# Optimization experiments

Measured on AMD Instinct MI355X. Metric: run time of the kernel, lower is better.

Reference implementation:

```python
import jax, jax.numpy as jnp
import numpy as np

N_NODES = 20000

def _gcn_conv(x, W, b, src, dst, n):
    # PyG GCNConv: add self-loops, symmetric normalization D^-1/2 (A+I) D^-1/2, then XW + b
    h = x @ W                                   # [n, out]
    loop = jnp.arange(n, dtype=src.dtype)
    s = jnp.concatenate([src, loop])            # sources incl. self-loops
    d = jnp.concatenate([dst, loop])            # targets incl. self-loops
    deg = jax.ops.segment_sum(jnp.ones_like(d, dtype=h.dtype), d, num_segments=n)
    dinv = jnp.where(deg > 0, jax.lax.rsqrt(deg), 0.0)
    norm = dinv[s] * dinv[d]                    # [E+n]
    msg = h[s] * norm[:, None]                  # gather + scale
    out = jax.ops.segment_sum(msg, d, num_segments=n)  # scatter-add
    return out + b


def setup_inputs() -> dict:
    key = jax.random.key(0)
    ks = jax.random.split(key, 12)
    n, text_dim, hidden, ncls = N_NODES, 768, 128, 4
    mel_flat = 128 * 128
    E = 640000
    def lin(k, fan_in, fan_out):
        bound = 1.0 / np.sqrt(fan_in)
        kw, kb = jax.random.split(k)
        W = jax.random.uniform(kw, (fan_in, fan_out), jnp.float32, -bound, bound)
        b = jax.random.uniform(kb, (fan_out,), jnp.float32, -bound, bound)
        return W, b
    W_mel, b_mel = lin(ks[0], mel_flat, hidden)
    W_cat, b_cat = lin(ks[1], text_dim + hidden, hidden)
    W1, b1 = lin(ks[2], hidden, hidden)
    W2, b2 = lin(ks[3], hidden, ncls)
    return {
        "text": jax.random.normal(ks[4], (n, text_dim), jnp.float32),
        "mel": jax.random.normal(ks[5], (n, 128, 128), jnp.float32),
        "edge_index": jax.random.randint(ks[6], (2, E), 0, n, jnp.int32),
        "W_mel": W_mel, "b_mel": b_mel,
        "W_cat": W_cat, "b_cat": b_cat,
        "W1": W1, "b1": b1,
        "W2": W2, "b2": b2,
    }


def reference(text, mel, edge_index, W_mel, b_mel, W_cat, b_cat, W1, b1, W2, b2):
    n = text.shape[0]
    src, dst = edge_index[0], edge_index[1]
    m = mel.reshape(n, -1)                      # flatten [N, 128*128]
    m = jax.nn.relu(m @ W_mel + b_mel)          # [N, hidden]
    x = jnp.concatenate([text, m], axis=1)      # [N, text_dim + hidden]
    x = jax.nn.relu(x @ W_cat + b_cat)          # [N, hidden]
    x = jax.nn.relu(_gcn_conv(x, W1, b1, src, dst, n))
    x = _gcn_conv(x, W2, b2, src, dst, n)       # [N, num_classes]
    return x
```

## Files before the change

### kernel.cpp

```cpp
#include <hip/hip_runtime.h>
#include <hip/hip_bf16.h>
#include <cstdint>

typedef float f32x4 __attribute__((ext_vector_type(4)));
typedef __bf16 bf16x8 __attribute__((ext_vector_type(8)));
typedef __bf16 bf16x4 __attribute__((ext_vector_type(4)));
typedef __bf16 bf16x2 __attribute__((ext_vector_type(2)));

#define HID 128

__global__ void pack_all(const float* __restrict__ Wa, const float* __restrict__ Wb,
                         const float* __restrict__ Wc,
                         __bf16* __restrict__ Ba, __bf16* __restrict__ Bb,
                         __bf16* __restrict__ Bc) {
    int idx = blockIdx.x * 256 + threadIdx.x;
    const int T1 = 512 * 512;
    const int T2 = 28 * 512;
    const int T3 = 4 * 512;
    const float* W; __bf16* B; int li;
    if (idx < T1)            { W = Wa; B = Ba; li = idx; }
    else if (idx < T1 + T2)  { W = Wb; B = Bb; li = idx - T1; }
    else if (idx < T1 + T2 + T3) { W = Wc; B = Bc; li = idx - T1 - T2; }
    else return;
    int lane = li & 63;
    int nf = (li >> 6) & 7;
    int ki = li >> 9;
    int n = nf * 16 + (lane & 15);
    int kb = ki * 32 + ((lane >> 4) * 8);
    bf16x8 v;
#pragma unroll
    for (int j = 0; j < 8; ++j) v[j] = (__bf16)W[(size_t)(kb + j) * HID + n];
    *reinterpret_cast<bf16x8*>(B + (size_t)li * 8) = v;
}

__global__ __launch_bounds__(256, 2) void gemm_mel_ks(
    const float* __restrict__ A0,
    const __bf16* __restrict__ Bf,
    float* __restrict__ part)
{
    const int tid = threadIdx.x;
    const int lane = tid & 63;
    const int wv = tid >> 6;
    const int quarter = blockIdx.x / 625;
    const int row_base = (blockIdx.x - quarter * 625) * 32;
    const int rif = lane & 15;
    const int kg = lane >> 4;
    const int s0 = quarter * 8;

    __shared__ __align__(16) char ldsb[65536];

    f32x4 zero = {0.f, 0.f, 0.f, 0.f};
    f32x4 acc[2][8];
#pragma unroll
    for (int i = 0; i < 2; ++i)
#pragma unroll
        for (int j = 0; j < 8; ++j) acc[i][j] = zero;

    const bf16x8* __restrict__ BfV = reinterpret_cast<const bf16x8*>(Bf);

    f32x4 st[16];

    auto stage_load = [&](int s) {
#pragma unroll
        for (int j = 0; j < 16; ++j) {
            int seg = wv * 16 + j;
            int row = seg >> 1, halfseg = seg & 1;
            const float* gp = A0 + (size_t)(row_base + row) * 16384 + s * 512 + halfseg * 256 + (lane << 2);
            st[j] = __builtin_nontemporal_load(reinterpret_cast<const f32x4*>(gp));
        }
    };
    auto stage_write = [&](int buf) {
#pragma unroll
        for (int j = 0; j < 16; ++j) {
            int seg = wv * 16 + j;
            int row = seg >> 1, halfseg = seg & 1;
            int byte = row * 1024 + ((halfseg * 512 + lane * 8) ^ ((row & 7) << 4)) + buf * 32768;
            bf16x4 v;
            v[0] = (__bf16)st[j][0]; v[1] = (__bf16)st[j][1];
            v[2] = (__bf16)st[j][2]; v[3] = (__bf16)st[j][3];
            *reinterpret_cast<bf16x4*>(ldsb + byte) = v;
        }
    };
    auto compute2 = [&](int cur, int s, int kt0) {
#pragma unroll
        for (int kt = kt0; kt < kt0 + 2; ++kt) {
            bf16x8 af[2];
#pragma unroll
            for (int mi = 0; mi < 2; ++mi) {
                int row = mi * 16 + rif;
                int byte = row * 1024 + ((wv * 256 + kt * 64 + kg * 16) ^ ((rif & 7) << 4)) + cur * 32768;
                af[mi] = *reinterpret_cast<const bf16x8*>(ldsb + byte);
            }
            int ki = s * 16 + wv * 4 + kt;
            const bf16x8* bp = BfV + (size_t)ki * 512 + lane;
#pragma unroll
            for (int nf = 0; nf < 8; ++nf) {
                bf16x8 b = bp[nf * 64];
                acc[0][nf] = __builtin_amdgcn_mfma_f32_16x16x32_bf16(af[0], b, acc[0][nf], 0, 0, 0);
                acc[1][nf] = __builtin_amdgcn_mfma_f32_16x16x32_bf16(af[1], b, acc[1][nf], 0, 0, 0);
            }
        }
    };

    stage_load(s0);
    stage_write(0);
    for (int t = 0; t < 8; ++t) {
        int s = s0 + t;
        int cur = t & 1;
        if (t + 1 < 8) stage_load(s + 1);
        __syncthreads();
        compute2(cur, s, 0);
        compute2(cur, s, 2);
        if (t + 1 < 8) stage_write(cur ^ 1);
    }

    __syncthreads();
    float* red = reinterpret_cast<float*>(ldsb);
#pragma unroll
    for (int mi = 0; mi < 2; ++mi)
#pragma unroll
        for (int nf = 0; nf < 8; ++nf)
#pragma unroll
            for (int j = 0; j < 4; ++j)
                red[(wv * 32 + mi * 16 + kg * 4 + j) * HID + nf * 16 + rif] = acc[mi][nf][j];
    __syncthreads();
    float* pb = part + (size_t)quarter * 20000 * HID;
#pragma unroll
    for (int p = 0; p < 16; ++p) {
        int idx = tid + p * 256;
        int r = idx >> 7, c = idx & 127;
        float v = red[r * HID + c] + red[(32 + r) * HID + c]
                + red[(64 + r) * HID + c] + red[(96 + r) * HID + c];
        pb[(size_t)(row_base + r) * HID + c] = v;
    }
}

__global__ void combine_m(const float* __restrict__ part, const float* __restrict__ bias,
                          __bf16* __restrict__ m) {
    int idx = blockIdx.x * 256 + threadIdx.x;
    const size_t N = (size_t)20000 * HID / 4;
    const f32x4* p = reinterpret_cast<const f32x4*>(part);
    f32x4 b = *reinterpret_cast<const f32x4*>(bias + (idx & 31) * 4);
    f32x4 v = p[idx] + p[idx + N] + p[idx + 2 * N] + p[idx + 3 * N] + b;
    bf16x4 r;
    r[0] = (__bf16)fmaxf(v.x, 0.f); r[1] = (__bf16)fmaxf(v.y, 0.f);
    r[2] = (__bf16)fmaxf(v.z, 0.f); r[3] = (__bf16)fmaxf(v.w, 0.f);
    *reinterpret_cast<bf16x4*>(m + (size_t)idx * 4) = r;
}

__global__ __launch_bounds__(256) void gemm_cat_h1(
    const float* __restrict__ A0,
    const __bf16* __restrict__ A1,
    const __bf16* __restrict__ Bf2,
    const __bf16* __restrict__ Bf3,
    const float* __restrict__ bcat,
    const float* __restrict__ dinv,
    __bf16* __restrict__ h1)
{
    const int tid = threadIdx.x;
    const int lane = tid & 63;
    const int w = tid >> 6;
    const int row_base = blockIdx.x * 32;
    const int rif = lane & 15;
    const int kg = lane >> 4;

    f32x4 zero = {0.f, 0.f, 0.f, 0.f};
    f32x4 acc[2][8];
#pragma unroll
    for (int i = 0; i < 2; ++i)
#pragma unroll
        for (int j = 0; j < 8; ++j) acc[i][j] = zero;

    const bf16x8* __restrict__ Bf2V = reinterpret_cast<const bf16x8*>(Bf2);
    const int kstart = w * 224;

#pragma unroll
    for (int it = 0; it < 7; ++it) {
        const int k0 = kstart + it * 32;
        const int kc = k0 + kg * 8;
        bf16x8 af[2];
#pragma unroll
        for (int mi = 0; mi < 2; ++mi) {
            const int row = row_base + mi * 16 + rif;
            if (k0 < 768) {
                const f32x4* apv = reinterpret_cast<const f32x4*>(A0 + (size_t)row * 768 + kc);
                f32x4 v0 = __builtin_nontemporal_load(apv);
                f32x4 v1 = __builtin_nontemporal_load(apv + 1);
                af[mi][0] = (__bf16)v0.x; af[mi][1] = (__bf16)v0.y;
                af[mi][2] = (__bf16)v0.z; af[mi][3] = (__bf16)v0.w;
                af[mi][4] = (__bf16)v1.x; af[mi][5] = (__bf16)v1.y;
                af[mi][6] = (__bf16)v1.z; af[mi][7] = (__bf16)v1.w;
            } else {
                af[mi] = *reinterpret_cast<const bf16x8*>(A1 + (size_t)row * HID + (kc - 768));
            }
        }
        const bf16x8* bp = Bf2V + (size_t)(k0 >> 5) * 512 + lane;
#pragma unroll
        for (int nf = 0; nf < 8; ++nf) {
            bf16x8 b = bp[nf * 64];
            acc[0][nf] = __builtin_amdgcn_mfma_f32_16x16x32_bf16(af[0], b, acc[0][nf], 0, 0, 0);
            acc[1][nf] = __builtin_amdgcn_mfma_f32_16x16x32_bf16(af[1], b, acc[1][nf], 0, 0, 0);
        }
    }

    __shared__ float red[4][32][HID];
    __shared__ __bf16 xs[32][136];

#pragma unroll
    for (int mi = 0; mi < 2; ++mi)
#pragma unroll
        for (int nf = 0; nf < 8; ++nf)
#pragma unroll
            for (int j = 0; j < 4; ++j)
                red[w][mi * 16 + kg * 4 + j][nf * 16 + rif] = acc[mi][nf][j];
    __syncthreads();
#pragma unroll
    for (int p = 0; p < 16; ++p) {
        int idx = tid + p * 256;
        int r = idx >> 7, c = idx & 127;
        float v = red[0][r][c] + red[1][r][c] + red[2][r][c] + red[3][r][c];
        v = fmaxf(v + bcat[c], 0.f);
        xs[r][c] = (__bf16)v;
    }
    __syncthreads();

    f32x4 acc2[2][8];
#pragma unroll
    for (int i = 0; i < 2; ++i)
#pragma unroll
        for (int j = 0; j < 8; ++j) acc2[i][j] = zero;

    {
        const int k0 = w * 32;
        bf16x8 af[2];
#pragma unroll
        for (int mi = 0; mi < 2; ++mi)
            af[mi] = *reinterpret_cast<const bf16x8*>(&xs[mi * 16 + rif][k0 + kg * 8]);
        const bf16x8* bp = reinterpret_cast<const bf16x8*>(Bf3) + (size_t)w * 512 + lane;
#pragma unroll
        for (int nf = 0; nf < 8; ++nf) {
            bf16x8 b = bp[nf * 64];
            acc2[0][nf] = __builtin_amdgcn_mfma_f32_16x16x32_bf16(af[0], b, acc2[0][nf], 0, 0, 0);
            acc2[1][nf] = __builtin_amdgcn_mfma_f32_16x16x32_bf16(af[1], b, acc2[1][nf], 0, 0, 0);
        }
    }

#pragma unroll
    for (int mi = 0; mi < 2; ++mi)
#pragma unroll
        for (int nf = 0; nf < 8; ++nf)
#pragma unroll
            for (int j = 0; j < 4; ++j)
                red[w][mi * 16 + kg * 4 + j][nf * 16 + rif] = acc2[mi][nf][j];
    __syncthreads();
#pragma unroll
    for (int p = 0; p < 16; ++p) {
        int idx = tid + p * 256;
        int r = idx >> 7, c = idx & 127;
        float v = red[0][r][c] + red[1][r][c] + red[2][r][c] + red[3][r][c];
        h1[(size_t)(row_base + r) * HID + c] = (__bf16)(v * dinv[row_base + r]);
    }
}

__global__ void count_dst(const int* __restrict__ dst, int* __restrict__ cnt, int E) {
    int e = blockIdx.x * 256 + threadIdx.x;
    if (e < E) atomicAdd(&cnt[dst[e]], 1);
}

__global__ __launch_bounds__(1024) void scan_block(const int* __restrict__ cnt,
    int* __restrict__ offs, float* __restrict__ dinv, int n) {
    int tid = threadIdx.x;
    int CH = (n + 1023) >> 10;
    int s0 = tid * CH;
    int s1 = min(s0 + CH, n);
    int sum = 0;
    for (int i = s0; i < s1; ++i) sum += cnt[i];
    int lane = tid & 63, wv = tid >> 6;
    int s = sum;
#pragma unroll
    for (int off = 1; off < 64; off <<= 1) {
        int t = __shfl_up(s, off);
        if (lane >= off) s += t;
    }
    __shared__ int wsum[16];
    __shared__ int wbase[16];
    if (lane == 63) wsum[wv] = s;
    __syncthreads();
    if (tid == 0) {
        int a = 0;
#pragma unroll
        for (int k = 0; k < 16; ++k) { wbase[k] = a; a += wsum[k]; }
    }
    __syncthreads();
    int run = wbase[wv] + (s - sum);
    for (int i = s0; i < s1; ++i) {
        int v = cnt[i];
        offs[i] = run;
        dinv[i] = rsqrtf((float)(v + 1));
        run += v;
    }
}

__global__ void fill_csr(const int* __restrict__ src, const int* __restrict__ dst,
                         const int* __restrict__ offs, int* __restrict__ fill,
                         int* __restrict__ srcs, int E) {
    int e = blockIdx.x * 256 + threadIdx.x;
    if (e >= E) return;
    int d = dst[e];
    int p = offs[d] + atomicAdd(&fill[d], 1);
    srcs[p] = src[e];
}

__global__ __launch_bounds__(64) void agg_h_w2(const __bf16* __restrict__ hs,
    const float* __restrict__ dinv, const int* __restrict__ offs,
    const int* __restrict__ cnt, const int* __restrict__ srcs,
    const float* __restrict__ b1, const float* __restrict__ W2,
    float* __restrict__ h2, int n) {
    int i = blockIdx.x;
    int c = threadIdx.x;
    float di = dinv[i];
    const int col = 2 * c;
    bf16x2 hv = *reinterpret_cast<const bf16x2*>(hs + (size_t)i * HID + col);
    float a0 = (float)hv[0];
    float a1 = (float)hv[1];
    int o = offs[i], e = cnt[i];
    int t = 0;
    for (; t + 4 <= e; t += 4) {
        int s0 = srcs[o + t], s1 = srcs[o + t + 1], s2 = srcs[o + t + 2], s3 = srcs[o + t + 3];
        bf16x2 v0 = *reinterpret_cast<const bf16x2*>(hs + (size_t)s0 * HID + col);
        bf16x2 v1 = *reinterpret_cast<const bf16x2*>(hs + (size_t)s1 * HID + col);
        bf16x2 v2 = *reinterpret_cast<const bf16x2*>(hs + (size_t)s2 * HID + col);
        bf16x2 v3 = *reinterpret_cast<const bf16x2*>(hs + (size_t)s3 * HID + col);
        a0 += (float)v0[0] + (float)v1[0] + (float)v2[0] + (float)v3[0];
        a1 += (float)v0[1] + (float)v1[1] + (float)v2[1] + (float)v3[1];
    }
    for (; t < e; ++t) {
        int s = srcs[o + t];
        bf16x2 v = *reinterpret_cast<const bf16x2*>(hs + (size_t)s * HID + col);
        a0 += (float)v[0];
        a1 += (float)v[1];
    }
    float yb0 = fmaxf(a0 * di + b1[col], 0.f);
    float yb1 = fmaxf(a1 * di + b1[col + 1], 0.f);
    float4 w0 = *reinterpret_cast<const float4*>(W2 + col * 4);
    float4 w1 = *reinterpret_cast<const float4*>(W2 + col * 4 + 4);
    float p0 = yb0 * w0.x + yb1 * w1.x;
    float p1 = yb0 * w0.y + yb1 * w1.y;
    float p2 = yb0 * w0.z + yb1 * w1.z;
    float p3 = yb0 * w0.w + yb1 * w1.w;
#pragma unroll
    for (int off = 32; off; off >>= 1) {
        p0 += __shfl_down(p0, off);
        p1 += __shfl_down(p1, off);
        p2 += __shfl_down(p2, off);
        p3 += __shfl_down(p3, off);
    }
    if (c == 0) {
        float4 r = {p0 * di, p1 * di, p2 * di, p3 * di};
        *reinterpret_cast<float4*>(h2 + (size_t)i * 4) = r;
    }
}

__global__ void agg4(const float* __restrict__ h2s, const float* __restrict__ dinv,
                     const int* __restrict__ offs, const int* __restrict__ cnt,
                     const int* __restrict__ srcs, const float* __restrict__ b2,
                     float* __restrict__ out, int n) {
    int gid = blockIdx.x * 256 + threadIdx.x;
    int i = gid >> 2;
    int c = gid & 3;
    if (i >= n) return;
    float di = dinv[i];
    float acc = h2s[(size_t)i * 4 + c];
    int o = offs[i], e = cnt[i];
    int t = 0;
    for (; t + 4 <= e; t += 4) {
        int a0 = srcs[o + t], a1 = srcs[o + t + 1], a2 = srcs[o + t + 2], a3 = srcs[o + t + 3];
        acc += h2s[(size_t)a0 * 4 + c] + h2s[(size_t)a1 * 4 + c]
             + h2s[(size_t)a2 * 4 + c] + h2s[(size_t)a3 * 4 + c];
    }
    for (; t < e; ++t) {
        int s = srcs[o + t];
        acc += h2s[(size_t)s * 4 + c];
    }
    out[(size_t)i * 4 + c] = acc * di + b2[c];
}

extern "C" void kernel_launch(void* const* d_in, const int* in_sizes, int n_in,
                              void* d_out, int out_size, void* d_ws, size_t ws_size,
                              hipStream_t stream) {
    const float* text = (const float*)d_in[0];
    const float* mel  = (const float*)d_in[1];
    const int*   ei   = (const int*)d_in[2];
    const float* Wmel = (const float*)d_in[3];
    const float* bmel = (const float*)d_in[4];
    const float* Wcat = (const float*)d_in[5];
    const float* bcat = (const float*)d_in[6];
    const float* W1   = (const float*)d_in[7];
    const float* b1   = (const float*)d_in[8];
    const float* W2   = (const float*)d_in[9];
    const float* b2   = (const float*)d_in[10];
    float* out = (float*)d_out;

    const int n = in_sizes[0] / 768;
    const int E = in_sizes[2] / 2;
    const int Kmel = 16384;

    char* ws = (char*)d_ws;
    size_t off = 0;
    auto alloc = [&](size_t bytes) {
        void* p = ws + off;
        off += (bytes + 255) & ~(size_t)255;
        return p;
    };
    __bf16* Bf1 = (__bf16*)alloc((size_t)Kmel * HID * 2);
    __bf16* Bf2 = (__bf16*)alloc((size_t)896 * HID * 2);
    __bf16* Bf3 = (__bf16*)alloc((size_t)HID * HID * 2);
    float* part = (float*)alloc((size_t)4 * n * HID * 4);
    __bf16* m   = (__bf16*)alloc((size_t)n * HID * 2);
    __bf16* h1  = (__bf16*)alloc((size_t)n * HID * 2);
    float* h2   = (float*)alloc((size_t)n * 4 * 4);
    int* cnt    = (int*)alloc((size_t)n * 4);
    int* offs   = (int*)alloc((size_t)n * 4);
    int* fill   = (int*)alloc((size_t)n * 4);
    float* dinv = (float*)alloc((size_t)n * 4);
    int* srcs   = (int*)alloc((size_t)E * 4);
    (void)ws_size; (void)n_in; (void)out_size;

    const int* srcI = ei;
    const int* dstI = ei + E;

    (void)hipMemsetAsync(cnt, 0, n * 4, stream);
    (void)hipMemsetAsync(fill, 0, n * 4, stream);
    count_dst<<<(E + 255) / 256, 256, 0, stream>>>(dstI, cnt, E);
    scan_block<<<1, 1024, 0, stream>>>(cnt, offs, dinv, n);
    fill_csr<<<(E + 255) / 256, 256, 0, stream>>>(srcI, dstI, offs, fill, srcs, E);

    pack_all<<<1088, 256, 0, stream>>>(Wmel, Wcat, W1, Bf1, Bf2, Bf3);

    gemm_mel_ks<<<2500, 256, 0, stream>>>(mel, Bf1, part);
    combine_m<<<(n * HID / 4) / 256, 256, 0, stream>>>(part, bmel, m);
    gemm_cat_h1<<<n / 32, 256, 0, stream>>>(text, m, Bf2, Bf3, bcat, dinv, h1);
    agg_h_w2<<<n, 64, 0, stream>>>(h1, dinv, offs, cnt, srcs, b1, W2, h2, n);
    agg4<<<(n * 4 + 255) / 256, 256, 0, stream>>>(h2, dinv, offs, cnt, srcs, b2, out, n);
}
```

Before: 455.0 us.

## Fuse split-K combine into cat GEMM, store bf16 partials, drop fill buffer

The mel GEMM now writes its four split-K partial sums as bf16 instead of fp32. The separate combine kernel is removed, and gemm_cat_h1 sums the partials, adds the bias and applies ReLU when it loads its A operand. The CSR build reuses the count array as a decrementing fill cursor and stores offs[n], so the memset for the fill buffer and the cnt reads in the aggregation kernels go away. The neighbour gather loop in agg_h_w2 is unrolled to 8 to keep more loads in flight. Rounding the partials to bf16 before summing adds some numerical error, and the cat GEMM now reads four partial buffers instead of one.

```diff
diff --git a/kernel.cpp b/kernel.cpp
--- a/kernel.cpp
+++ b/kernel.cpp
@@ -36,7 +36,7 @@
 __global__ __launch_bounds__(256, 2) void gemm_mel_ks(
     const float* __restrict__ A0,
     const __bf16* __restrict__ Bf,
-    float* __restrict__ part)
+    __bf16* __restrict__ part)
 {
     const int tid = threadIdx.x;
     const int lane = tid & 63;
@@ -124,33 +124,27 @@
             for (int j = 0; j < 4; ++j)
                 red[(wv * 32 + mi * 16 + kg * 4 + j) * HID + nf * 16 + rif] = acc[mi][nf][j];
     __syncthreads();
-    float* pb = part + (size_t)quarter * 20000 * HID;
-#pragma unroll
-    for (int p = 0; p < 16; ++p) {
+    __bf16* pb = part + (size_t)quarter * 20000 * HID;
+#pragma unroll
+    for (int p = 0; p < 8; ++p) {
         int idx = tid + p * 256;
-        int r = idx >> 7, c = idx & 127;
-        float v = red[r * HID + c] + red[(32 + r) * HID + c]
-                + red[(64 + r) * HID + c] + red[(96 + r) * HID + c];
-        pb[(size_t)(row_base + r) * HID + c] = v;
-    }
-}
-
-__global__ void combine_m(const float* __restrict__ part, const float* __restrict__ bias,
-                          __bf16* __restrict__ m) {
-    int idx = blockIdx.x * 256 + threadIdx.x;
-    const size_t N = (size_t)20000 * HID / 4;
-    const f32x4* p = reinterpret_cast<const f32x4*>(part);
-    f32x4 b = *reinterpret_cast<const f32x4*>(bias + (idx & 31) * 4);
-    f32x4 v = p[idx] + p[idx + N] + p[idx + 2 * N] + p[idx + 3 * N] + b;
-    bf16x4 r;
-    r[0] = (__bf16)fmaxf(v.x, 0.f); r[1] = (__bf16)fmaxf(v.y, 0.f);
-    r[2] = (__bf16)fmaxf(v.z, 0.f); r[3] = (__bf16)fmaxf(v.w, 0.f);
-    *reinterpret_cast<bf16x4*>(m + (size_t)idx * 4) = r;
+        int r = idx >> 6;
+        int c2 = (idx & 63) * 2;
+        float v0 = red[r * HID + c2]     + red[(32 + r) * HID + c2]
+                 + red[(64 + r) * HID + c2] + red[(96 + r) * HID + c2];
+        float v1 = red[r * HID + c2 + 1] + red[(32 + r) * HID + c2 + 1]
+                 + red[(64 + r) * HID + c2 + 1] + red[(96 + r) * HID + c2 + 1];
+        union { bf16x2 h; unsigned int u; } cv;
+        cv.h[0] = (__bf16)v0; cv.h[1] = (__bf16)v1;
+        __builtin_nontemporal_store(cv.u,
+            reinterpret_cast<unsigned int*>(pb + (size_t)(row_base + r) * HID + c2));
+    }
 }
 
 __global__ __launch_bounds__(256) void gemm_cat_h1(
     const float* __restrict__ A0,
-    const __bf16* __restrict__ A1,
+    const __bf16* __restrict__ part,
+    const float* __restrict__ bmel,
     const __bf16* __restrict__ Bf2,
     const __bf16* __restrict__ Bf3,
     const float* __restrict__ bcat,
@@ -173,6 +167,7 @@
 
     const bf16x8* __restrict__ Bf2V = reinterpret_cast<const bf16x8*>(Bf2);
     const int kstart = w * 224;
+    const size_t N = (size_t)20000 * HID;
 
 #pragma unroll
     for (int it = 0; it < 7; ++it) {
@@ -191,7 +186,18 @@
                 af[mi][4] = (__bf16)v1.x; af[mi][5] = (__bf16)v1.y;
                 af[mi][6] = (__bf16)v1.z; af[mi][7] = (__bf16)v1.w;
             } else {
-                af[mi] = *reinterpret_cast<const bf16x8*>(A1 + (size_t)row * HID + (kc - 768));
+                const int mcol = kc - 768;
+                const size_t base = (size_t)row * HID + mcol;
+                bf16x8 q0 = *reinterpret_cast<const bf16x8*>(part + base);
+                bf16x8 q1 = *reinterpret_cast<const bf16x8*>(part + N + base);
+                bf16x8 q2 = *reinterpret_cast<const bf16x8*>(part + 2 * N + base);
+                bf16x8 q3 = *reinterpret_cast<const bf16x8*>(part + 3 * N + base);
+                const float* bp_ = bmel + mcol;
+#pragma unroll
+                for (int jj = 0; jj < 8; ++jj) {
+                    float v = (float)q0[jj] + (float)q1[jj] + (float)q2[jj] + (float)q3[jj] + bp_[jj];
+                    af[mi][jj] = (__bf16)fmaxf(v, 0.f);
+                }
             }
         }
         const bf16x8* bp = Bf2V + (size_t)(k0 >> 5) * 512 + lane;
@@ -290,6 +296,7 @@
         int a = 0;
 #pragma unroll
         for (int k = 0; k < 16; ++k) { wbase[k] = a; a += wsum[k]; }
+        offs[n] = a;
     }
     __syncthreads();
     int run = wbase[wv] + (s - sum);
@@ -302,18 +309,18 @@
 }
 
 __global__ void fill_csr(const int* __restrict__ src, const int* __restrict__ dst,
-                         const int* __restrict__ offs, int* __restrict__ fill,
+                         const int* __restrict__ offs, int* __restrict__ cnt,
                          int* __restrict__ srcs, int E) {
     int e = blockIdx.x * 256 + threadIdx.x;
     if (e >= E) return;
     int d = dst[e];
-    int p = offs[d] + atomicAdd(&fill[d], 1);
+    int p = offs[d] + atomicAdd(&cnt[d], -1) - 1;
     srcs[p] = src[e];
 }
 
 __global__ __launch_bounds__(64) void agg_h_w2(const __bf16* __restrict__ hs,
     const float* __restrict__ dinv, const int* __restrict__ offs,
-    const int* __restrict__ cnt, const int* __restrict__ srcs,
+    const int* __restrict__ srcs,
     const float* __restrict__ b1, const float* __restrict__ W2,
     float* __restrict__ h2, int n) {
     int i = blockIdx.x;
@@ -323,16 +330,18 @@
     bf16x2 hv = *reinterpret_cast<const bf16x2*>(hs + (size_t)i * HID + col);
     float a0 = (float)hv[0];
     float a1 = (float)hv[1];
-    int o = offs[i], e = cnt[i];
+    int o = offs[i];
+    int e = offs[i + 1] - o;
     int t = 0;
-    for (; t + 4 <= e; t += 4) {
-        int s0 = srcs[o + t], s1 = srcs[o + t + 1], s2 = srcs[o + t + 2], s3 = srcs[o + t + 3];
-        bf16x2 v0 = *reinterpret_cast<const bf16x2*>(hs + (size_t)s0 * HID + col);
-        bf16x2 v1 = *reinterpret_cast<const bf16x2*>(hs + (size_t)s1 * HID + col);
-        bf16x2 v2 = *reinterpret_cast<const bf16x2*>(hs + (size_t)s2 * HID + col);
-        bf16x2 v3 = *reinterpret_cast<const bf16x2*>(hs + (size_t)s3 * HID + col);
-        a0 += (float)v0[0] + (float)v1[0] + (float)v2[0] + (float)v3[0];
-        a1 += (float)v0[1] + (float)v1[1] + (float)v2[1] + (float)v3[1];
+    for (; t + 8 <= e; t += 8) {
+        int sx[8];
+#pragma unroll
+        for (int q = 0; q < 8; ++q) sx[q] = srcs[o + t + q];
+        bf16x2 v[8];
+#pragma unroll
+        for (int q = 0; q < 8; ++q) v[q] = *reinterpret_cast<const bf16x2*>(hs + (size_t)sx[q] * HID + col);
+#pragma unroll
+        for (int q = 0; q < 8; ++q) { a0 += (float)v[q][0]; a1 += (float)v[q][1]; }
     }
     for (; t < e; ++t) {
         int s = srcs[o + t];
@@ -362,7 +371,7 @@
 }
 
 __global__ void agg4(const float* __restrict__ h2s, const float* __restrict__ dinv,
-                     const int* __restrict__ offs, const int* __restrict__ cnt,
+                     const int* __restrict__ offs,
                      const int* __restrict__ srcs, const float* __restrict__ b2,
                      float* __restrict__ out, int n) {
     int gid = blockIdx.x * 256 + threadIdx.x;
@@ -371,7 +380,8 @@
     if (i >= n) return;
     float di = dinv[i];
     float acc = h2s[(size_t)i * 4 + c];
-    int o = offs[i], e = cnt[i];
+    int o = offs[i];
+    int e = offs[i + 1] - o;
     int t = 0;
     for (; t + 4 <= e; t += 4) {
         int a0 = srcs[o + t], a1 = srcs[o + t + 1], a2 = srcs[o + t + 2], a3 = srcs[o + t + 3];
@@ -415,13 +425,11 @@
     __bf16* Bf1 = (__bf16*)alloc((size_t)Kmel * HID * 2);
     __bf16* Bf2 = (__bf16*)alloc((size_t)896 * HID * 2);
     __bf16* Bf3 = (__bf16*)alloc((size_t)HID * HID * 2);
-    float* part = (float*)alloc((size_t)4 * n * HID * 4);
-    __bf16* m   = (__bf16*)alloc((size_t)n * HID * 2);
+    __bf16* part = (__bf16*)alloc((size_t)4 * n * HID * 2);
     __bf16* h1  = (__bf16*)alloc((size_t)n * HID * 2);
     float* h2   = (float*)alloc((size_t)n * 4 * 4);
     int* cnt    = (int*)alloc((size_t)n * 4);
-    int* offs   = (int*)alloc((size_t)n * 4);
-    int* fill   = (int*)alloc((size_t)n * 4);
+    int* offs   = (int*)alloc((size_t)(n + 1) * 4);
     float* dinv = (float*)alloc((size_t)n * 4);
     int* srcs   = (int*)alloc((size_t)E * 4);
     (void)ws_size; (void)n_in; (void)out_size;
@@ -430,16 +438,14 @@
     const int* dstI = ei + E;
 
     (void)hipMemsetAsync(cnt, 0, n * 4, stream);
-    (void)hipMemsetAsync(fill, 0, n * 4, stream);
     count_dst<<<(E + 255) / 256, 256, 0, stream>>>(dstI, cnt, E);
     scan_block<<<1, 1024, 0, stream>>>(cnt, offs, dinv, n);
-    fill_csr<<<(E + 255) / 256, 256, 0, stream>>>(srcI, dstI, offs, fill, srcs, E);
+    fill_csr<<<(E + 255) / 256, 256, 0, stream>>>(srcI, dstI, offs, cnt, srcs, E);
 
     pack_all<<<1088, 256, 0, stream>>>(Wmel, Wcat, W1, Bf1, Bf2, Bf3);
 
     gemm_mel_ks<<<2500, 256, 0, stream>>>(mel, Bf1, part);
-    combine_m<<<(n * HID / 4) / 256, 256, 0, stream>>>(part, bmel, m);
-    gemm_cat_h1<<<n / 32, 256, 0, stream>>>(text, m, Bf2, Bf3, bcat, dinv, h1);
-    agg_h_w2<<<n, 64, 0, stream>>>(h1, dinv, offs, cnt, srcs, b1, W2, h2, n);
-    agg4<<<(n * 4 + 255) / 256, 256, 0, stream>>>(h2, dinv, offs, cnt, srcs, b2, out, n);
-}
+    gemm_cat_h1<<<n / 32, 256, 0, stream>>>(text, part, bmel, Bf2, Bf3, bcat, dinv, h1);
+    agg_h_w2<<<n, 64, 0, stream>>>(h1, dinv, offs, srcs, b1, W2, h2, n);
+    agg4<<<(n * 4 + 255) / 256, 256, 0, stream>>>(h2, dinv, offs, srcs, b2, out, n);
+}
```

After: 435.4 us. 4.3% less time.
